# Optimization experiments

Hardware: AMD Instinct MI355X
Metric: run time of the kernel (lower is better)

Reference implementation:

```python
import jax, jax.numpy as jnp
import numpy as np

B, K, FM, TS, H, W = 128, 24, 24, 11, 40, 40
EPS = 1e-6


def setup_inputs() -> dict:
    key = jax.random.key(0)
    ks = jax.random.split(key, 8)

    def w(k, shape):
        fan_in = float(np.prod(shape[2:]))
        return jax.random.normal(k, shape, jnp.float32) / np.float32(np.sqrt(fan_in))

    return {
        "x": jax.random.normal(ks[0], (B, 1, H, W), jnp.float32),
        "noise": jax.random.uniform(ks[1], (B, K), jnp.float32, -2.0, 2.0),
        "W1": w(ks[2], (K, 128, 1, 3, 3)), "b1": jnp.zeros((K, 128), jnp.float32),
        "W2": w(ks[3], (K, 128, 128, 3, 3)), "b2": jnp.zeros((K, 128), jnp.float32),
        "W3": w(ks[4], (K, 128, 128, 3, 3)), "b3": jnp.zeros((K, 128), jnp.float32),
        "W4": w(ks[5], (K, 128, 128, 3, 3)), "b4": jnp.zeros((K, 128), jnp.float32),
        "W5": w(ks[6], (K, FM, 128, 1, 1)), "b5": jnp.zeros((K, FM), jnp.float32),
        "templates": jax.random.normal(ks[7], (K, TS, TS), jnp.float32),
    }


def _conv(x, w, b, s):
    y = jax.lax.conv_general_dilated(x, w, (s, s), 'VALID',
                                     dimension_numbers=('NCHW', 'OIHW', 'NCHW'))
    return y + b[None, :, None, None]


def _inv_affine_mats(pose):
    # pose [B,K,6]: angle(deg), tx, ty, scale, shear_x(deg), shear_y(deg)
    # torchvision-style inverse affine matrix (maps output canvas coords -> template coords)
    ang = jnp.deg2rad(pose[..., 0])
    tx, ty = pose[..., 1], pose[..., 2]
    sc = pose[..., 3] + EPS
    sx = jnp.deg2rad(pose[..., 4])
    sy = jnp.deg2rad(pose[..., 5])
    a = jnp.cos(ang - sy) / jnp.cos(sy)
    b = -jnp.cos(ang - sy) * jnp.tan(sx) / jnp.cos(sy) - jnp.sin(ang)
    c = jnp.sin(ang - sy) / jnp.cos(sy)
    d = -jnp.sin(ang - sy) * jnp.tan(sx) / jnp.cos(sy) + jnp.cos(ang)
    m00, m01, m10, m11 = d / sc, -b / sc, -c / sc, a / sc
    cx = cy = (TS - 1) * 0.5
    m02 = m00 * (-cx - tx) + m01 * (-cy - ty) + cx
    m12 = m10 * (-cx - tx) + m11 * (-cy - ty) + cy
    return m00, m01, m02, m10, m11, m12


def _warp_templates(templates, pose):
    # Fused affine warp + resize-to-(H,W), bilinear, zero fill (batched grid_sample).
    m00, m01, m02, m10, m11, m12 = _inv_affine_mats(pose)  # each [B,K]
    ys, xs = jnp.meshgrid(jnp.arange(H, dtype=jnp.float32),
                          jnp.arange(W, dtype=jnp.float32), indexing='ij')
    u = (xs + 0.5) * (TS / W) - 0.5  # output pixel -> template-canvas x
    v = (ys + 0.5) * (TS / H) - 0.5
    src_x = m00[..., None, None] * u + m01[..., None, None] * v + m02[..., None, None]
    src_y = m10[..., None, None] * u + m11[..., None, None] * v + m12[..., None, None]

    def sample(tmpl, sx_, sy_):  # tmpl [TS,TS]; sx_,sy_ [B,H,W]
        x0 = jnp.floor(sx_); y0 = jnp.floor(sy_)
        wx = sx_ - x0; wy = sy_ - y0
        x0i = x0.astype(jnp.int32); y0i = y0.astype(jnp.int32)

        def tap(yi, xi):
            ok = (xi >= 0) & (xi < TS) & (yi >= 0) & (yi < TS)
            val = tmpl[jnp.clip(yi, 0, TS - 1), jnp.clip(xi, 0, TS - 1)]
            return jnp.where(ok, val, 0.0)

        v00 = tap(y0i, x0i); v01 = tap(y0i, x0i + 1)
        v10 = tap(y0i + 1, x0i); v11 = tap(y0i + 1, x0i + 1)
        return (v00 * (1 - wx) + v01 * wx) * (1 - wy) + (v10 * (1 - wx) + v11 * wx) * wy

    return jax.vmap(sample, in_axes=(0, 1, 1), out_axes=1)(templates, src_x, src_y)  # [B,K,H,W]


def _forward(x, noise, W1, b1, W2, b2, W3, b3, W4, b4, W5, b5, templates):
    def capsule(w1, bb1, w2, bb2, w3, bb3, w4, bb4, w5, bb5):
        h = jax.nn.relu(_conv(x, w1, bb1, 2))
        h = jax.nn.relu(_conv(h, w2, bb2, 2))
        h = jax.nn.relu(_conv(h, w3, bb3, 1))
        h = jax.nn.relu(_conv(h, w4, bb4, 1))
        return _conv(h, w5, bb5, 1)

    outs = jax.vmap(capsule)(W1, b1, W2, b2, W3, b3, W4, b4, W5, b5)  # [K,B,FM,h,w]
    att = outs[:, :, -1]  # [K,B,h,w]
    hs, ws = att.shape[-2:]
    att = jax.nn.softmax(att.reshape(K, B, hs * ws), axis=-1).reshape(K, B, hs, ws)
    pooled = jnp.einsum('kbfhw,kbhw->bkf', outs[:, :, :-1], att)  # [B,K,FM-1]

    x_m = jax.nn.relu(pooled[:, :, :6])                        # [B,K,6] pose
    d_m = jax.nn.sigmoid(pooled[:, :, 6] + noise)[..., None]   # [B,K,1] presence
    c_z = jax.nn.relu(pooled[:, :, 7:])                        # [B,K,16]

    tt = _warp_templates(templates, x_m)                       # [B,K,H,W]
    mix_prob = jax.nn.softmax(d_m * tt.reshape(B, K, H * W), axis=2).reshape(B, K, H, W)

    std = jnp.std(x.reshape(B, 1, -1), axis=-1, ddof=1)[:, None]   # [B,1,1] (unbiased, as torch)
    mult = (1.0 / jnp.sqrt(std * 2.0 * jnp.pi))[..., None]         # [B,1,1,1] (as written in source)
    pmul = (-1.0 / (2.0 * std ** 2))[..., None]                    # [B,1,1,1]
    xd = jax.lax.stop_gradient(x)                                  # detach_x = x.data
    gaussians = mult * jnp.exp((xd - tt) ** 2 * pmul)              # [B,K,H,W]
    ll = jnp.log(jnp.sum(gaussians * mix_prob, axis=1)).sum((-1, -2)).mean()

    x_m_det = jax.lax.stop_gradient(x_m)
    d_m_det = jax.lax.stop_gradient(d_m)
    tmpl_det = jnp.broadcast_to(jax.lax.stop_gradient(templates).reshape(1, K, TS * TS),
                                (B, K, TS * TS))
    input_ocae = jnp.concatenate([d_m_det, x_m_det, tmpl_det, c_z], axis=-1)  # [B,K,144]
    return ll, input_ocae, x_m_det, d_m_det


def reference(x, noise, W1, b1, W2, b2, W3, b3, W4, b4, W5, b5, templates):
    return _forward(x, noise, W1, b1, W2, b2, W3, b3, W4, b4, W5, b5, templates)
```

## Files before the change

kernel.cpp:

```cpp
#include <hip/hip_runtime.h>
#include <math.h>

typedef __attribute__((ext_vector_type(8))) short bf16x8;
typedef __attribute__((ext_vector_type(4))) float f32x4;
typedef unsigned int uint32;
typedef unsigned short ushort;

namespace {
constexpr int KK = 24, BB = 128;

constexpr size_t SZ_W1P = (size_t)24 * 128 * 32 * 2;
constexpr size_t SZ_W5P = (size_t)24 * 32 * 128 * 2;
constexpr size_t SZ_WB  = (size_t)24 * 128 * 1152 * 2;
constexpr size_t OFF_W1P = 0;
constexpr size_t OFF_W5P = OFF_W1P + SZ_W1P;
constexpr size_t OFF_WB2 = OFF_W5P + SZ_W5P;
constexpr size_t OFF_WB3 = OFF_WB2 + SZ_WB;
constexpr size_t OFF_WB4 = OFF_WB3 + SZ_WB;
constexpr size_t OFF_TT  = OFF_WB4 + SZ_WB;
constexpr size_t SZ_TT   = (size_t)128 * 24 * 1600 * 2;
constexpr size_t OFF_SMAX = OFF_TT + SZ_TT;
constexpr size_t OFF_SDEN = OFF_SMAX + 12288;
constexpr size_t OFF_DM   = OFF_SDEN + 12288;
constexpr size_t OFF_PART = OFF_DM + 12288;

constexpr long long O_OCAE = 1;
constexpr long long O_XM   = O_OCAE + (long long)BB * KK * 144;
constexpr long long O_DM   = O_XM + (long long)BB * KK * 6;

constexpr int R1_SZ   = 80864;
constexpr int XIM_OFF = 0;
constexpr int H1T_OFF = 23104;
constexpr int XSB_OFF = 74464;
constexpr int H2S_OFF = 0;
constexpr int H3S_OFF = 0;
constexpr int H4B_OFF = 31392;
constexpr int OUTS_OFF = 0;
constexpr int ATT_OFF = 4800;
constexpr int PS_OFF  = 5000;
}

__device__ inline ushort f2bf(float f) {
  uint32 u = __builtin_bit_cast(uint32, f);
  u += 0x7fffu + ((u >> 16) & 1u);
  return (ushort)(u >> 16);
}
__device__ inline float bf2f(ushort u) {
  return __builtin_bit_cast(float, (uint32)u << 16);
}
__device__ inline uint32 cvtpk(float a, float b) {
  uint32 r;
  asm("v_cvt_pk_bf16_f32 %0, %1, %2" : "=v"(r) : "v"(a), "v"(b));
  return r;
}

__global__ __launch_bounds__(128) void k_w1p(const float* __restrict__ W1,
                                             const float* __restrict__ W5,
                                             ushort* __restrict__ W1p,
                                             ushort* __restrict__ W5p) {
  const int k = blockIdx.x, t = threadIdx.x;
  {
    ushort tmp[32];
    #pragma unroll
    for (int i = 0; i < 32; ++i) tmp[i] = 0;
    #pragma unroll
    for (int j = 0; j < 9; ++j) tmp[j] = f2bf(W1[(k * 128 + t) * 9 + j]);
    uint4* dp = (uint4*)(W1p + ((size_t)k * 128 + t) * 32);
    #pragma unroll
    for (int i = 0; i < 4; ++i) dp[i] = ((uint4*)tmp)[i];
  }
  if (t < 32) {
    ushort* dp = W5p + ((size_t)k * 32 + t) * 128;
    if (t < 24) {
      const float* sp = W5 + (size_t)k * 3072 + t * 128;
      for (int ci = 0; ci < 128; ++ci) dp[ci] = f2bf(sp[ci]);
    } else {
      for (int ci = 0; ci < 128; ++ci) dp[ci] = 0;
    }
  }
}

__global__ __launch_bounds__(256) void k_wp(
    const float* __restrict__ W2, const float* __restrict__ W3, const float* __restrict__ W4,
    ushort* __restrict__ W2p, ushort* __restrict__ W3p, ushort* __restrict__ W4p) {
  const int blk = blockIdx.x;
  const int sel = blk / 384;
  const int bb = blk - sel * 384;
  const float* src = (sel == 0) ? W2 : (sel == 1) ? W3 : W4;
  ushort* dst = (sel == 0) ? W2p : (sel == 1) ? W3p : W4p;
  const int k = bb >> 4;
  const int co = ((bb & 15) << 3) + (threadIdx.x >> 5);
  const int cil = threadIdx.x & 31;
  #pragma unroll
  for (int c = 0; c < 4; ++c) {
    const float* sp = src + ((size_t)(k * 128 + co) * 128 + c * 32 + cil) * 9;
    float v[9];
    #pragma unroll
    for (int j = 0; j < 9; ++j) v[j] = sp[j];
    ushort* dp = dst + (size_t)(k * 4 + c) * 9 * 128 * 32;
    #pragma unroll
    for (int j = 0; j < 9; ++j) dp[(j * 128 + co) * 32 + cil] = f2bf(v[j]);
  }
}

__device__ inline float tapf(const float* tm, int yi, int xi) {
  const bool ok = (xi >= 0) & (xi < 11) & (yi >= 0) & (yi < 11);
  const int yc = min(max(yi, 0), 10), xc = min(max(xi, 0), 10);
  const float v = tm[yc * 11 + xc];
  return ok ? v : 0.0f;
}

__global__ __launch_bounds__(256, 2) void k_tower(
    const float* __restrict__ x, const ushort* __restrict__ W1p, const float* __restrict__ b1,
    const ushort* __restrict__ W2p, const float* __restrict__ b2,
    const ushort* __restrict__ W3p, const float* __restrict__ b3,
    const ushort* __restrict__ W4p, const float* __restrict__ b4,
    const ushort* __restrict__ W5p, const float* __restrict__ b5,
    const float* __restrict__ noise, const float* __restrict__ templates,
    float* __restrict__ out, ushort* __restrict__ ttb,
    float* __restrict__ smax, float* __restrict__ sden, float* __restrict__ dmw)
{
  const int bi = blockIdx.x;
  const int blk = (bi & 7) * 192 + (bi >> 3);
  const int kb0 = blk * 2;
  const int k = kb0 >> 7;
  const int b0 = kb0 & 127;
  const int t = threadIdx.x;

  __shared__ __align__(16) char R1[R1_SZ];
  __shared__ float red[8];
  __shared__ float b5s[24];
  __shared__ float tm[121];

  ushort* xim = (ushort*)(R1 + XIM_OFF);
  ushort* h1T = (ushort*)(R1 + H1T_OFF);
  ushort* xsb = (ushort*)(R1 + XSB_OFF);
  ushort* h2s = (ushort*)(R1 + H2S_OFF);
  ushort* h3s = (ushort*)(R1 + H3S_OFF);
  ushort* h4b = (ushort*)(R1 + H4B_OFF);
  float*  outs_s = (float*)(R1 + OUTS_OFF);
  float*  att_s  = (float*)(R1 + ATT_OFF);
  float*  ps  = (float*)(R1 + PS_OFF);

  for (int i = t; i < 800; i += 256) {
    const int im = i / 400, j = i - im * 400;
    const float4 v = ((const float4*)(x + (size_t)(b0 + im) * 1600))[j];
    uint2 pk;
    pk.x = cvtpk(v.x, v.y);
    pk.y = cvtpk(v.z, v.w);
    *(uint2*)(xsb + im * 1600 + 4 * j) = pk;
  }
  __syncthreads();

  for (int f = t; f < 722; f += 256) {
    const int im = f / 361, fl = f - im * 361;
    const int py = fl / 19, px = fl - 19 * py;
    const ushort* bp = xsb + im * 1600 + py * 80 + px * 2;
    const uint32 t0 = bp[0], t1 = bp[1], t2 = bp[2];
    const uint32 t3 = bp[40], t4 = bp[41], t5 = bp[42];
    const uint32 t6 = bp[80], t7 = bp[81], t8 = bp[82];
    uint4* dp = (uint4*)(xim + (im * 361 + fl) * 16);
    dp[0] = make_uint4(t0 | (t1 << 16), t2 | (t3 << 16), t4 | (t5 << 16), t6 | (t7 << 16));
    dp[1] = make_uint4(t8, 0u, 0u, 0u);
  }

  const int w = t >> 6, lane = t & 63, r = lane & 15, s = lane >> 4;
  const int img = w >> 1;
  const int wi  = w & 1;
  const int m0  = wi * 64;

  ushort* xim_i = xim + img * 5776;
  ushort* h1T_i = h1T + img * 14440;
  ushort* h2s_i = h2s + img * 12960;
  ushort* h3s_i = h3s + img * 7840;
  ushort* h4b_i = h4b + img * 3400;

  {
    int pb[6]; bool vld[6];
    #pragma unroll
    for (int ni = 0; ni < 6; ++ni) {
      const int n = 16 * ni + r;
      const int py = n / 9, px = n - 9 * py;
      pb[ni] = 38 * py + 2 * px;
      vld[ni] = (n < 81);
    }

    f32x4 acc[4][6];
    #pragma unroll
    for (int mi = 0; mi < 4; ++mi)
      #pragma unroll
      for (int ni = 0; ni < 6; ++ni) acc[mi][ni] = (f32x4){0.f, 0.f, 0.f, 0.f};

    for (int c = 0; c < 4; ++c) {
      __syncthreads();
      {
        const bf16x8 a1 = *(const bf16x8*)(W1p + ((size_t)k * 128 + 32 * c + 16 * wi + r) * 32 + 8 * s);
        const int cil0 = 16 * wi + 4 * s;
        const float4 b1v = *(const float4*)(b1 + k * 128 + 32 * c + cil0);
        const bf16x8 bz = {};
        for (int nt = 0; nt < 23; ++nt) {
          const int n = nt * 16 + r;
          const int pos = (n < 361) ? n : 360;
          bf16x8 bv = *(const bf16x8*)(xim_i + pos * 16 + 8 * (s & 1));
          if (s >= 2) bv = bz;
          f32x4 cc = __builtin_amdgcn_mfma_f32_16x16x32_bf16(a1, bv, (f32x4){0.f, 0.f, 0.f, 0.f}, 0, 0, 0);
          if (n < 361) {
            uint2 pk;
            pk.x = cvtpk(fmaxf(cc[0] + b1v.x, 0.f), fmaxf(cc[1] + b1v.y, 0.f));
            pk.y = cvtpk(fmaxf(cc[2] + b1v.z, 0.f), fmaxf(cc[3] + b1v.w, 0.f));
            *(uint2*)(h1T_i + n * 40 + cil0) = pk;
          }
        }
      }
      __syncthreads();
      const ushort* Abase = W2p + ((((size_t)k * 4 + c) * 9) * 128 + m0 + r) * 32 + 8 * s;
      bf16x8 Ab[2][4];
      #pragma unroll
      for (int mi = 0; mi < 4; ++mi) Ab[0][mi] = *(const bf16x8*)(Abase + mi * 512);
      #pragma unroll
      for (int j = 0; j < 9; ++j) {
        if (j < 8) {
          #pragma unroll
          for (int mi = 0; mi < 4; ++mi)
            Ab[(j + 1) & 1][mi] = *(const bf16x8*)(Abase + (size_t)(j + 1) * 4096 + mi * 512);
        }
        const int off = (j / 3) * 19 + (j - 3 * (j / 3));
        bf16x8 Bv[6];
        #pragma unroll
        for (int ni = 0; ni < 6; ++ni) {
          const int pos = vld[ni] ? pb[ni] + off : 0;
          Bv[ni] = *(const bf16x8*)(h1T_i + pos * 40 + 8 * s);
        }
        #pragma unroll
        for (int mi = 0; mi < 4; ++mi)
          #pragma unroll
          for (int ni = 0; ni < 6; ++ni)
            acc[mi][ni] = __builtin_amdgcn_mfma_f32_16x16x32_bf16(Ab[j & 1][mi], Bv[ni], acc[mi][ni], 0, 0, 0);
      }
    }
    __syncthreads();
    #pragma unroll
    for (int mi = 0; mi < 4; ++mi) {
      const int co0 = m0 + 16 * mi + 4 * s;
      const float4 bv = *(const float4*)(b2 + k * 128 + co0);
      const int c2 = co0 >> 5, cil = co0 & 31;
      #pragma unroll
      for (int ni = 0; ni < 6; ++ni) {
        const int p = 16 * ni + r;
        if (p < 81) {
          uint2 pk;
          pk.x = cvtpk(fmaxf(acc[mi][ni][0] + bv.x, 0.f), fmaxf(acc[mi][ni][1] + bv.y, 0.f));
          pk.y = cvtpk(fmaxf(acc[mi][ni][2] + bv.z, 0.f), fmaxf(acc[mi][ni][3] + bv.w, 0.f));
          *(uint2*)(h2s_i + (c2 * 81 + p) * 40 + cil) = pk;
        }
      }
    }
  }
  __syncthreads();

  {
    int pb[4]; bool vld[4];
    #pragma unroll
    for (int ni = 0; ni < 4; ++ni) {
      const int n = 16 * ni + r;
      const int py = n / 7, px = n - 7 * py;
      pb[ni] = (9 * py + px) * 40;
      vld[ni] = (n < 49);
    }
    f32x4 acc[4][4];
    #pragma unroll
    for (int mi = 0; mi < 4; ++mi)
      #pragma unroll
      for (int ni = 0; ni < 4; ++ni) acc[mi][ni] = (f32x4){0.f, 0.f, 0.f, 0.f};

    for (int c = 0; c < 4; ++c) {
      const ushort* Abase = W3p + ((((size_t)k * 4 + c) * 9) * 128 + m0 + r) * 32 + 8 * s;
      bf16x8 Ab[2][4];
      #pragma unroll
      for (int mi = 0; mi < 4; ++mi) Ab[0][mi] = *(const bf16x8*)(Abase + mi * 512);
      #pragma unroll
      for (int j = 0; j < 9; ++j) {
        if (j < 8) {
          #pragma unroll
          for (int mi = 0; mi < 4; ++mi)
            Ab[(j + 1) & 1][mi] = *(const bf16x8*)(Abase + (size_t)(j + 1) * 4096 + mi * 512);
        }
        const int off40 = ((j / 3) * 9 + (j - 3 * (j / 3))) * 40;
        bf16x8 Bv[4];
        #pragma unroll
        for (int ni = 0; ni < 4; ++ni) {
          const int pos40 = vld[ni] ? pb[ni] : 0;
          Bv[ni] = *(const bf16x8*)(h2s_i + c * 3240 + pos40 + off40 + 8 * s);
        }
        #pragma unroll
        for (int mi = 0; mi < 4; ++mi)
          #pragma unroll
          for (int ni = 0; ni < 4; ++ni)
            acc[mi][ni] = __builtin_amdgcn_mfma_f32_16x16x32_bf16(Ab[j & 1][mi], Bv[ni], acc[mi][ni], 0, 0, 0);
      }
    }
    __syncthreads();
    #pragma unroll
    for (int mi = 0; mi < 4; ++mi) {
      const int co0 = m0 + 16 * mi + 4 * s;
      const float4 bv = *(const float4*)(b3 + k * 128 + co0);
      const int c2 = co0 >> 5, cil = co0 & 31;
      #pragma unroll
      for (int ni = 0; ni < 4; ++ni) {
        const int p = 16 * ni + r;
        if (p < 49) {
          uint2 pk;
          pk.x = cvtpk(fmaxf(acc[mi][ni][0] + bv.x, 0.f), fmaxf(acc[mi][ni][1] + bv.y, 0.f));
          pk.y = cvtpk(fmaxf(acc[mi][ni][2] + bv.z, 0.f), fmaxf(acc[mi][ni][3] + bv.w, 0.f));
          *(uint2*)(h3s_i + (c2 * 49 + p) * 40 + cil) = pk;
        }
      }
    }
    for (int i = t; i < 121; i += 256) tm[i] = templates[k * 121 + i];
  }
  __syncthreads();

  {
    int pb[2]; bool vld[2];
    #pragma unroll
    for (int ni = 0; ni < 2; ++ni) {
      const int n = 16 * ni + r;
      const int py = n / 5, px = n - 5 * py;
      pb[ni] = (7 * py + px) * 40;
      vld[ni] = (n < 25);
    }
    f32x4 acc[4][2];
    #pragma unroll
    for (int mi = 0; mi < 4; ++mi)
      #pragma unroll
      for (int ni = 0; ni < 2; ++ni) acc[mi][ni] = (f32x4){0.f, 0.f, 0.f, 0.f};

    for (int c = 0; c < 4; ++c) {
      const ushort* Abase = W4p + ((((size_t)k * 4 + c) * 9) * 128 + m0 + r) * 32 + 8 * s;
      bf16x8 Ab[2][4];
      #pragma unroll
      for (int mi = 0; mi < 4; ++mi) Ab[0][mi] = *(const bf16x8*)(Abase + mi * 512);
      #pragma unroll
      for (int j = 0; j < 9; ++j) {
        if (j < 8) {
          #pragma unroll
          for (int mi = 0; mi < 4; ++mi)
            Ab[(j + 1) & 1][mi] = *(const bf16x8*)(Abase + (size_t)(j + 1) * 4096 + mi * 512);
        }
        const int off40 = ((j / 3) * 7 + (j - 3 * (j / 3))) * 40;
        bf16x8 Bv[2];
        #pragma unroll
        for (int ni = 0; ni < 2; ++ni) {
          const int pos40 = vld[ni] ? pb[ni] : 0;
          Bv[ni] = *(const bf16x8*)(h3s_i + c * 1960 + pos40 + off40 + 8 * s);
        }
        #pragma unroll
        for (int mi = 0; mi < 4; ++mi)
          #pragma unroll
          for (int ni = 0; ni < 2; ++ni)
            acc[mi][ni] = __builtin_amdgcn_mfma_f32_16x16x32_bf16(Ab[j & 1][mi], Bv[ni], acc[mi][ni], 0, 0, 0);
      }
    }
    __syncthreads();
    #pragma unroll
    for (int mi = 0; mi < 4; ++mi) {
      const int co0 = m0 + 16 * mi + 4 * s;
      const float4 bv = *(const float4*)(b4 + k * 128 + co0);
      #pragma unroll
      for (int ni = 0; ni < 2; ++ni) {
        const int p = 16 * ni + r;
        if (p < 25) {
          uint2 pk;
          pk.x = cvtpk(fmaxf(acc[mi][ni][0] + bv.x, 0.f), fmaxf(acc[mi][ni][1] + bv.y, 0.f));
          pk.y = cvtpk(fmaxf(acc[mi][ni][2] + bv.z, 0.f), fmaxf(acc[mi][ni][3] + bv.w, 0.f));
          *(uint2*)(h4b_i + p * 136 + co0) = pk;
        }
      }
    }
    if (t < 24) b5s[t] = b5[k * 24 + t];
  }
  __syncthreads();

  {
    const int mt = wi;
    f32x4 acc5[2];
    acc5[0] = (f32x4){0.f, 0.f, 0.f, 0.f};
    acc5[1] = (f32x4){0.f, 0.f, 0.f, 0.f};
    const ushort* A5 = W5p + ((size_t)k * 32 + mt * 16 + r) * 128 + 8 * s;
    #pragma unroll
    for (int ks = 0; ks < 4; ++ks) {
      const bf16x8 a5 = *(const bf16x8*)(A5 + ks * 32);
      #pragma unroll
      for (int nt = 0; nt < 2; ++nt) {
        const int p = 16 * nt + r;
        const int pv = (p < 25) ? p : 0;
        const bf16x8 bv = *(const bf16x8*)(h4b_i + pv * 136 + ks * 32 + 8 * s);
        acc5[nt] = __builtin_amdgcn_mfma_f32_16x16x32_bf16(a5, bv, acc5[nt], 0, 0, 0);
      }
    }
    #pragma unroll
    for (int nt = 0; nt < 2; ++nt) {
      const int p = 16 * nt + r;
      if (p < 25) {
        #pragma unroll
        for (int rg = 0; rg < 4; ++rg) {
          const int fm = mt * 16 + 4 * s + rg;
          if (fm < 24) outs_s[img * 600 + fm * 25 + p] = acc5[nt][rg] + b5s[fm];
        }
      }
    }
  }
  __syncthreads();

  if (!(t & 64)) {
    const int im = t >> 7;
    const int tl = t & 63;
    float v = (tl < 25) ? outs_s[im * 600 + 575 + tl] : -1e30f;
    #pragma unroll
    for (int off = 32; off; off >>= 1) v = fmaxf(v, __shfl_xor(v, off));
    const float m = v;
    float e = (tl < 25) ? expf(outs_s[im * 600 + 575 + tl] - m) : 0.0f;
    float ss = e;
    #pragma unroll
    for (int off = 32; off; off >>= 1) ss += __shfl_xor(ss, off);
    if (tl < 25) att_s[im * 25 + tl] = e / ss;
  }
  __syncthreads();

  {
    const int im = t >> 7;
    const int tl = t & 127;
    if (tl < 23) {
      float v = 0.f;
      #pragma unroll
      for (int p = 0; p < 25; ++p) v = fmaf(outs_s[im * 600 + tl * 25 + p], att_s[im * 25 + p], v);
      ps[im * 23 + tl] = v;
    }
  }
  __syncthreads();

  float dmv[2];
  #pragma unroll
  for (int im = 0; im < 2; ++im) {
    const int idx = (b0 + im) * KK + k;
    const float dl = ps[im * 23 + 6] + noise[idx];
    dmv[im] = 1.0f / (1.0f + expf(-dl));
  }

  #pragma unroll
  for (int im = 0; im < 2; ++im) {
    const int idx = (b0 + im) * KK + k;
    if (t < 144) {
      float v;
      if (t == 0)       v = dmv[im];
      else if (t < 7)   v = fmaxf(ps[im * 23 + t - 1], 0.0f);
      else if (t < 128) v = tm[t - 7];
      else              v = fmaxf(ps[im * 23 + 7 + (t - 128)], 0.0f);
      out[O_OCAE + (size_t)idx * 144 + t] = v;
    }
    if (t < 6) out[O_XM + (size_t)idx * 6 + t] = fmaxf(ps[im * 23 + t], 0.0f);
    if (t == 0) out[O_DM + idx] = dmv[im];
  }

  const int im = t >> 7;
  const int tl = t & 127;
  const int idx = (b0 + im) * KK + k;
  const float dm = dmv[im];

  const float D2R = 0.017453292519943295f;
  const float ang = fmaxf(ps[im * 23 + 0], 0.0f) * D2R;
  const float tx = fmaxf(ps[im * 23 + 1], 0.0f), ty = fmaxf(ps[im * 23 + 2], 0.0f);
  const float sc = fmaxf(ps[im * 23 + 3], 0.0f) + 1e-6f;
  const float sxr = fmaxf(ps[im * 23 + 4], 0.0f) * D2R;
  const float syr = fmaxf(ps[im * 23 + 5], 0.0f) * D2R;
  const float cas = cosf(ang - syr), sas = sinf(ang - syr);
  const float csy = cosf(syr), tsx = tanf(sxr);
  const float a_ = cas / csy;
  const float b_ = -cas * tsx / csy - sinf(ang);
  const float c_ = sas / csy;
  const float d_ = -sas * tsx / csy + cosf(ang);
  const float m00 = d_ / sc, m01 = -b_ / sc, m10 = -c_ / sc, m11 = a_ / sc;
  const float m02 = m00 * (-5.0f - tx) + m01 * (-5.0f - ty) + 5.0f;
  const float m12 = m10 * (-5.0f - tx) + m11 * (-5.0f - ty) + 5.0f;

  const float S = 0.275f;
  float ttv[13];
  float lmax = -1e30f;
  #pragma unroll
  for (int i = 0; i < 13; ++i) {
    const int pix = tl + 128 * i;
    float val2 = 0.0f;
    if (pix < 1600) {
      const int py = pix / 40, px = pix - 40 * py;
      const float u = (px + 0.5f) * S - 0.5f;
      const float v = (py + 0.5f) * S - 0.5f;
      const float sx = m00 * u + m01 * v + m02;
      const float sy = m10 * u + m11 * v + m12;
      const float x0 = floorf(sx), y0 = floorf(sy);
      const float wx = sx - x0, wy = sy - y0;
      const int xi = (int)x0, yi = (int)y0;
      const float v00 = tapf(tm, yi, xi);
      const float v01 = tapf(tm, yi, xi + 1);
      const float v10 = tapf(tm, yi + 1, xi);
      const float v11 = tapf(tm, yi + 1, xi + 1);
      const float val = (v00 * (1.0f - wx) + v01 * wx) * (1.0f - wy) + (v10 * (1.0f - wx) + v11 * wx) * wy;
      const ushort tb = f2bf(val);
      val2 = bf2f(tb);
      ttb[(size_t)idx * 1600 + pix] = tb;
      lmax = fmaxf(lmax, dm * val2);
    }
    ttv[i] = val2;
  }

  #pragma unroll
  for (int off = 32; off; off >>= 1) lmax = fmaxf(lmax, __shfl_xor(lmax, off));
  if ((t & 63) == 0) red[t >> 6] = lmax;
  __syncthreads();
  const float m = fmaxf(red[2 * im], red[2 * im + 1]);
  float ls = 0.0f;
  #pragma unroll
  for (int i = 0; i < 13; ++i)
    if (tl + 128 * i < 1600) ls += expf(fmaf(dm, ttv[i], -m));
  #pragma unroll
  for (int off = 32; off; off >>= 1) ls += __shfl_xor(ls, off);
  __syncthreads();
  if ((t & 63) == 0) red[4 + (t >> 6)] = ls;
  __syncthreads();
  if ((t & 127) == 0) {
    smax[idx] = m;
    sden[idx] = red[4 + 2 * im] + red[5 + 2 * im];
    dmw[idx] = dm;
  }
}

__global__ __launch_bounds__(256) void k_ll(
    const float* __restrict__ x, const ushort* __restrict__ ttb,
    const float* __restrict__ smax, const float* __restrict__ sden,
    const float* __restrict__ dmw, float* __restrict__ part)
{
  const int b = blockIdx.x >> 2;
  const int chunk = blockIdx.x & 3;
  const int t = threadIdx.x;

  __shared__ __align__(16) float xs[1600];
  __shared__ float kd[24], km[24], ki[24];
  __shared__ float red[4], red2[4];

  for (int i = t; i < 400; i += 256)
    ((float4*)xs)[i] = ((const float4*)(x + (size_t)b * 1600))[i];
  if (t < 24) {
    kd[t] = dmw[b * 24 + t];
    km[t] = smax[b * 24 + t];
    ki[t] = 1.0f / sden[b * 24 + t];
  }
  __syncthreads();

  float s1 = 0.f, s2 = 0.f;
  for (int i = t; i < 1600; i += 256) { const float v = xs[i]; s1 += v; s2 = fmaf(v, v, s2); }
  #pragma unroll
  for (int off = 32; off; off >>= 1) { s1 += __shfl_xor(s1, off); s2 += __shfl_xor(s2, off); }
  if ((t & 63) == 0) { red[t >> 6] = s1; red2[t >> 6] = s2; }
  __syncthreads();
  s1 = red[0] + red[1] + red[2] + red[3];
  s2 = red2[0] + red2[1] + red2[2] + red2[3];
  const float var = (s2 - s1 * s1 * (1.0f / 1600.0f)) * (1.0f / 1599.0f);
  const float stdv = sqrtf(var);
  const float mult = 1.0f / sqrtf(stdv * 6.283185307179586f);
  const float pmul = -1.0f / (2.0f * stdv * stdv);

  const int p0 = chunk * 400;
  float ll = 0.0f;
  for (int ii = t; ii < 400; ii += 256) {
    const int pix = p0 + ii;
    const float xv = xs[pix];
    float sum = 0.0f;
    #pragma unroll 6
    for (int kk2 = 0; kk2 < 24; ++kk2) {
      const float tv = bf2f(ttb[(size_t)(b * 24 + kk2) * 1600 + pix]);
      const float dxv = xv - tv;
      sum += expf(fmaf(dxv * dxv, pmul, fmaf(kd[kk2], tv, -km[kk2]))) * ki[kk2];
    }
    ll += logf(mult * sum);
  }
  #pragma unroll
  for (int off = 32; off; off >>= 1) ll += __shfl_xor(ll, off);
  __syncthreads();
  if ((t & 63) == 0) red[t >> 6] = ll;
  __syncthreads();
  if (t == 0) part[blockIdx.x] = red[0] + red[1] + red[2] + red[3];
}

__global__ void k_final(const float* __restrict__ part, float* __restrict__ out)
{
  const int t = threadIdx.x;
  float v = part[t] + part[t + 256];
  #pragma unroll
  for (int off = 32; off; off >>= 1) v += __shfl_xor(v, off);
  __shared__ float red[4];
  if ((t & 63) == 0) red[t >> 6] = v;
  __syncthreads();
  if (t == 0) out[0] = (red[0] + red[1] + red[2] + red[3]) * (1.0f / 128.0f);
}

extern "C" void kernel_launch(void* const* d_in, const int* in_sizes, int n_in,
                              void* d_out, int out_size, void* d_ws, size_t ws_size,
                              hipStream_t stream)
{
  const float* x     = (const float*)d_in[0];
  const float* noise = (const float*)d_in[1];
  const float* W1    = (const float*)d_in[2];
  const float* b1    = (const float*)d_in[3];
  const float* W2    = (const float*)d_in[4];
  const float* b2    = (const float*)d_in[5];
  const float* W3    = (const float*)d_in[6];
  const float* b3    = (const float*)d_in[7];
  const float* W4    = (const float*)d_in[8];
  const float* b4    = (const float*)d_in[9];
  const float* W5    = (const float*)d_in[10];
  const float* b5    = (const float*)d_in[11];
  const float* tmpl  = (const float*)d_in[12];
  float* out = (float*)d_out;
  char* wsb = (char*)d_ws;

  ushort* W1p = (ushort*)(wsb + OFF_W1P);
  ushort* W5p = (ushort*)(wsb + OFF_W5P);
  ushort* W2p = (ushort*)(wsb + OFF_WB2);
  ushort* W3p = (ushort*)(wsb + OFF_WB3);
  ushort* W4p = (ushort*)(wsb + OFF_WB4);
  ushort* ttp  = (ushort*)(wsb + OFF_TT);
  float* smaxp = (float*)(wsb + OFF_SMAX);
  float* sdenp = (float*)(wsb + OFF_SDEN);
  float* dmp   = (float*)(wsb + OFF_DM);
  float* partp = (float*)(wsb + OFF_PART);

  k_w1p<<<24, 128, 0, stream>>>(W1, W5, W1p, W5p);
  k_wp<<<1152, 256, 0, stream>>>(W2, W3, W4, W2p, W3p, W4p);
  k_tower<<<KK * BB / 2, 256, 0, stream>>>(x, W1p, b1, W2p, b2, W3p, b3, W4p, b4,
                                           W5p, b5, noise, tmpl, out, ttp, smaxp, sdenp, dmp);
  k_ll<<<BB * 4, 256, 0, stream>>>(x, ttp, smaxp, sdenp, dmp, partp);
  k_final<<<1, 256, 0, stream>>>(partp, out);
}
```

Before: 271.4 us.

## Split tower kernel N-dimension across twice as many waves per block

Doubles k_tower's block size from 256 to 512 threads. Each image is now handled by four waves, split across output channels and across spatial tiles, instead of two, so per-wave accumulator and B-fragment counts halve across the conv2–conv5 MFMA stages. MFMA bursts are also wrapped with s_setprio to favour matrix issue. The intent is more latency hiding and better occupancy. In exchange, every wave reloads the same A (weight) fragments, adding redundant global/L2 traffic, and the reductions gain extra synchronisation.

```diff
diff --git a/kernel.cpp b/kernel.cpp
--- a/kernel.cpp
+++ b/kernel.cpp
@@ -110,7 +110,7 @@
   return ok ? v : 0.0f;
 }
 
-__global__ __launch_bounds__(256, 2) void k_tower(
+__global__ __launch_bounds__(512, 4) void k_tower(
     const float* __restrict__ x, const ushort* __restrict__ W1p, const float* __restrict__ b1,
     const ushort* __restrict__ W2p, const float* __restrict__ b2,
     const ushort* __restrict__ W3p, const float* __restrict__ b3,
@@ -128,7 +128,7 @@
   const int t = threadIdx.x;
 
   __shared__ __align__(16) char R1[R1_SZ];
-  __shared__ float red[8];
+  __shared__ float red[16];
   __shared__ float b5s[24];
   __shared__ float tm[121];
 
@@ -142,7 +142,7 @@
   float*  att_s  = (float*)(R1 + ATT_OFF);
   float*  ps  = (float*)(R1 + PS_OFF);
 
-  for (int i = t; i < 800; i += 256) {
+  for (int i = t; i < 800; i += 512) {
     const int im = i / 400, j = i - im * 400;
     const float4 v = ((const float4*)(x + (size_t)(b0 + im) * 1600))[j];
     uint2 pk;
@@ -152,7 +152,7 @@
   }
   __syncthreads();
 
-  for (int f = t; f < 722; f += 256) {
+  for (int f = t; f < 722; f += 512) {
     const int im = f / 361, fl = f - im * 361;
     const int py = fl / 19, px = fl - 19 * py;
     const ushort* bp = xsb + im * 1600 + py * 80 + px * 2;
@@ -165,8 +165,10 @@
   }
 
   const int w = t >> 6, lane = t & 63, r = lane & 15, s = lane >> 4;
-  const int img = w >> 1;
-  const int wi  = w & 1;
+  const int img = w >> 2;
+  const int sub = w & 3;
+  const int wi  = sub & 1;
+  const int nj  = sub >> 1;
   const int m0  = wi * 64;
 
   ushort* xim_i = xim + img * 5776;
@@ -176,20 +178,20 @@
   ushort* h4b_i = h4b + img * 3400;
 
   {
-    int pb[6]; bool vld[6];
-    #pragma unroll
-    for (int ni = 0; ni < 6; ++ni) {
-      const int n = 16 * ni + r;
+    int pb[3]; bool vld[3];
+    #pragma unroll
+    for (int ni = 0; ni < 3; ++ni) {
+      const int n = nj * 48 + 16 * ni + r;
       const int py = n / 9, px = n - 9 * py;
       pb[ni] = 38 * py + 2 * px;
       vld[ni] = (n < 81);
     }
 
-    f32x4 acc[4][6];
+    f32x4 acc[4][3];
     #pragma unroll
     for (int mi = 0; mi < 4; ++mi)
       #pragma unroll
-      for (int ni = 0; ni < 6; ++ni) acc[mi][ni] = (f32x4){0.f, 0.f, 0.f, 0.f};
+      for (int ni = 0; ni < 3; ++ni) acc[mi][ni] = (f32x4){0.f, 0.f, 0.f, 0.f};
 
     for (int c = 0; c < 4; ++c) {
       __syncthreads();
@@ -198,7 +200,8 @@
         const int cil0 = 16 * wi + 4 * s;
         const float4 b1v = *(const float4*)(b1 + k * 128 + 32 * c + cil0);
         const bf16x8 bz = {};
-        for (int nt = 0; nt < 23; ++nt) {
+        const int nt0 = nj ? 12 : 0, nt1 = nj ? 23 : 12;
+        for (int nt = nt0; nt < nt1; ++nt) {
           const int n = nt * 16 + r;
           const int pos = (n < 361) ? n : 360;
           bf16x8 bv = *(const bf16x8*)(xim_i + pos * 16 + 8 * (s & 1));
@@ -225,17 +228,19 @@
             Ab[(j + 1) & 1][mi] = *(const bf16x8*)(Abase + (size_t)(j + 1) * 4096 + mi * 512);
         }
         const int off = (j / 3) * 19 + (j - 3 * (j / 3));
-        bf16x8 Bv[6];
+        bf16x8 Bv[3];
         #pragma unroll
-        for (int ni = 0; ni < 6; ++ni) {
+        for (int ni = 0; ni < 3; ++ni) {
           const int pos = vld[ni] ? pb[ni] + off : 0;
           Bv[ni] = *(const bf16x8*)(h1T_i + pos * 40 + 8 * s);
         }
+        __builtin_amdgcn_s_setprio(1);
         #pragma unroll
         for (int mi = 0; mi < 4; ++mi)
           #pragma unroll
-          for (int ni = 0; ni < 6; ++ni)
+          for (int ni = 0; ni < 3; ++ni)
             acc[mi][ni] = __builtin_amdgcn_mfma_f32_16x16x32_bf16(Ab[j & 1][mi], Bv[ni], acc[mi][ni], 0, 0, 0);
+        __builtin_amdgcn_s_setprio(0);
       }
     }
     __syncthreads();
@@ -245,8 +250,8 @@
       const float4 bv = *(const float4*)(b2 + k * 128 + co0);
       const int c2 = co0 >> 5, cil = co0 & 31;
       #pragma unroll
-      for (int ni = 0; ni < 6; ++ni) {
-        const int p = 16 * ni + r;
+      for (int ni = 0; ni < 3; ++ni) {
+        const int p = nj * 48 + 16 * ni + r;
         if (p < 81) {
           uint2 pk;
           pk.x = cvtpk(fmaxf(acc[mi][ni][0] + bv.x, 0.f), fmaxf(acc[mi][ni][1] + bv.y, 0.f));
@@ -259,19 +264,19 @@
   __syncthreads();
 
   {
-    int pb[4]; bool vld[4];
-    #pragma unroll
-    for (int ni = 0; ni < 4; ++ni) {
-      const int n = 16 * ni + r;
+    int pb[2]; bool vld[2];
+    #pragma unroll
+    for (int ni = 0; ni < 2; ++ni) {
+      const int n = nj * 32 + 16 * ni + r;
       const int py = n / 7, px = n - 7 * py;
       pb[ni] = (9 * py + px) * 40;
       vld[ni] = (n < 49);
     }
-    f32x4 acc[4][4];
+    f32x4 acc[4][2];
     #pragma unroll
     for (int mi = 0; mi < 4; ++mi)
       #pragma unroll
-      for (int ni = 0; ni < 4; ++ni) acc[mi][ni] = (f32x4){0.f, 0.f, 0.f, 0.f};
+      for (int ni = 0; ni < 2; ++ni) acc[mi][ni] = (f32x4){0.f, 0.f, 0.f, 0.f};
 
     for (int c = 0; c < 4; ++c) {
       const ushort* Abase = W3p + ((((size_t)k * 4 + c) * 9) * 128 + m0 + r) * 32 + 8 * s;
@@ -286,17 +291,19 @@
             Ab[(j + 1) & 1][mi] = *(const bf16x8*)(Abase + (size_t)(j + 1) * 4096 + mi * 512);
         }
         const int off40 = ((j / 3) * 9 + (j - 3 * (j / 3))) * 40;
-        bf16x8 Bv[4];
+        bf16x8 Bv[2];
         #pragma unroll
-        for (int ni = 0; ni < 4; ++ni) {
+        for (int ni = 0; ni < 2; ++ni) {
           const int pos40 = vld[ni] ? pb[ni] : 0;
           Bv[ni] = *(const bf16x8*)(h2s_i + c * 3240 + pos40 + off40 + 8 * s);
         }
+        __builtin_amdgcn_s_setprio(1);
         #pragma unroll
         for (int mi = 0; mi < 4; ++mi)
           #pragma unroll
-          for (int ni = 0; ni < 4; ++ni)
+          for (int ni = 0; ni < 2; ++ni)
             acc[mi][ni] = __builtin_amdgcn_mfma_f32_16x16x32_bf16(Ab[j & 1][mi], Bv[ni], acc[mi][ni], 0, 0, 0);
+        __builtin_amdgcn_s_setprio(0);
       }
     }
     __syncthreads();
@@ -306,8 +313,8 @@
       const float4 bv = *(const float4*)(b3 + k * 128 + co0);
       const int c2 = co0 >> 5, cil = co0 & 31;
       #pragma unroll
-      for (int ni = 0; ni < 4; ++ni) {
-        const int p = 16 * ni + r;
+      for (int ni = 0; ni < 2; ++ni) {
+        const int p = nj * 32 + 16 * ni + r;
         if (p < 49) {
           uint2 pk;
           pk.x = cvtpk(fmaxf(acc[mi][ni][0] + bv.x, 0.f), fmaxf(acc[mi][ni][1] + bv.y, 0.f));
@@ -316,24 +323,17 @@
         }
       }
     }
-    for (int i = t; i < 121; i += 256) tm[i] = templates[k * 121 + i];
+    if (t < 121) tm[t] = templates[k * 121 + t];
   }
   __syncthreads();
 
   {
-    int pb[2]; bool vld[2];
-    #pragma unroll
-    for (int ni = 0; ni < 2; ++ni) {
-      const int n = 16 * ni + r;
-      const int py = n / 5, px = n - 5 * py;
-      pb[ni] = (7 * py + px) * 40;
-      vld[ni] = (n < 25);
-    }
-    f32x4 acc[4][2];
-    #pragma unroll
-    for (int mi = 0; mi < 4; ++mi)
-      #pragma unroll
-      for (int ni = 0; ni < 2; ++ni) acc[mi][ni] = (f32x4){0.f, 0.f, 0.f, 0.f};
+    const int n4 = nj * 16 + r;
+    const int py4 = n4 / 5, px4 = n4 - 5 * py4;
+    const int pb4 = (n4 < 25) ? (7 * py4 + px4) * 40 : 0;
+    f32x4 acc[4];
+    #pragma unroll
+    for (int mi = 0; mi < 4; ++mi) acc[mi] = (f32x4){0.f, 0.f, 0.f, 0.f};
 
     for (int c = 0; c < 4; ++c) {
       const ushort* Abase = W4p + ((((size_t)k * 4 + c) * 9) * 128 + m0 + r) * 32 + 8 * s;
@@ -348,17 +348,12 @@
             Ab[(j + 1) & 1][mi] = *(const bf16x8*)(Abase + (size_t)(j + 1) * 4096 + mi * 512);
         }
         const int off40 = ((j / 3) * 7 + (j - 3 * (j / 3))) * 40;
-        bf16x8 Bv[2];
-        #pragma unroll
-        for (int ni = 0; ni < 2; ++ni) {
-          const int pos40 = vld[ni] ? pb[ni] : 0;
-          Bv[ni] = *(const bf16x8*)(h3s_i + c * 1960 + pos40 + off40 + 8 * s);
-        }
+        const bf16x8 bv = *(const bf16x8*)(h3s_i + c * 1960 + pb4 + off40 + 8 * s);
+        __builtin_amdgcn_s_setprio(1);
         #pragma unroll
         for (int mi = 0; mi < 4; ++mi)
-          #pragma unroll
-          for (int ni = 0; ni < 2; ++ni)
-            acc[mi][ni] = __builtin_amdgcn_mfma_f32_16x16x32_bf16(Ab[j & 1][mi], Bv[ni], acc[mi][ni], 0, 0, 0);
+          acc[mi] = __builtin_amdgcn_mfma_f32_16x16x32_bf16(Ab[j & 1][mi], bv, acc[mi], 0, 0, 0);
+        __builtin_amdgcn_s_setprio(0);
       }
     }
     __syncthreads();
@@ -366,15 +361,12 @@
     for (int mi = 0; mi < 4; ++mi) {
       const int co0 = m0 + 16 * mi + 4 * s;
       const float4 bv = *(const float4*)(b4 + k * 128 + co0);
-      #pragma unroll
-      for (int ni = 0; ni < 2; ++ni) {
-        const int p = 16 * ni + r;
-        if (p < 25) {
-          uint2 pk;
-          pk.x = cvtpk(fmaxf(acc[mi][ni][0] + bv.x, 0.f), fmaxf(acc[mi][ni][1] + bv.y, 0.f));
-          pk.y = cvtpk(fmaxf(acc[mi][ni][2] + bv.z, 0.f), fmaxf(acc[mi][ni][3] + bv.w, 0.f));
-          *(uint2*)(h4b_i + p * 136 + co0) = pk;
-        }
+      const int p = nj * 16 + r;
+      if (p < 25) {
+        uint2 pk;
+        pk.x = cvtpk(fmaxf(acc[mi][0] + bv.x, 0.f), fmaxf(acc[mi][1] + bv.y, 0.f));
+        pk.y = cvtpk(fmaxf(acc[mi][2] + bv.z, 0.f), fmaxf(acc[mi][3] + bv.w, 0.f));
+        *(uint2*)(h4b_i + p * 136 + co0) = pk;
       }
     }
     if (t < 24) b5s[t] = b5[k * 24 + t];
@@ -382,54 +374,43 @@
   __syncthreads();
 
   {
-    const int mt = wi;
-    f32x4 acc5[2];
-    acc5[0] = (f32x4){0.f, 0.f, 0.f, 0.f};
-    acc5[1] = (f32x4){0.f, 0.f, 0.f, 0.f};
-    const ushort* A5 = W5p + ((size_t)k * 32 + mt * 16 + r) * 128 + 8 * s;
+    f32x4 acc5 = (f32x4){0.f, 0.f, 0.f, 0.f};
+    const ushort* A5 = W5p + ((size_t)k * 32 + wi * 16 + r) * 128 + 8 * s;
+    const int p = nj * 16 + r;
+    const int pv = (p < 25) ? p : 0;
     #pragma unroll
     for (int ks = 0; ks < 4; ++ks) {
       const bf16x8 a5 = *(const bf16x8*)(A5 + ks * 32);
-      #pragma unroll
-      for (int nt = 0; nt < 2; ++nt) {
-        const int p = 16 * nt + r;
-        const int pv = (p < 25) ? p : 0;
-        const bf16x8 bv = *(const bf16x8*)(h4b_i + pv * 136 + ks * 32 + 8 * s);
-        acc5[nt] = __builtin_amdgcn_mfma_f32_16x16x32_bf16(a5, bv, acc5[nt], 0, 0, 0);
-      }
-    }
-    #pragma unroll
-    for (int nt = 0; nt < 2; ++nt) {
-      const int p = 16 * nt + r;
-      if (p < 25) {
-        #pragma unroll
-        for (int rg = 0; rg < 4; ++rg) {
-          const int fm = mt * 16 + 4 * s + rg;
-          if (fm < 24) outs_s[img * 600 + fm * 25 + p] = acc5[nt][rg] + b5s[fm];
-        }
-      }
-    }
-  }
-  __syncthreads();
-
-  if (!(t & 64)) {
-    const int im = t >> 7;
-    const int tl = t & 63;
-    float v = (tl < 25) ? outs_s[im * 600 + 575 + tl] : -1e30f;
+      const bf16x8 bv = *(const bf16x8*)(h4b_i + pv * 136 + ks * 32 + 8 * s);
+      acc5 = __builtin_amdgcn_mfma_f32_16x16x32_bf16(a5, bv, acc5, 0, 0, 0);
+    }
+    if (p < 25) {
+      #pragma unroll
+      for (int rg = 0; rg < 4; ++rg) {
+        const int fm = wi * 16 + 4 * s + rg;
+        if (fm < 24) outs_s[img * 600 + fm * 25 + p] = acc5[rg] + b5s[fm];
+      }
+    }
+  }
+  __syncthreads();
+
+  if (sub == 0) {
+    const int im = img;
+    float v = (lane < 25) ? outs_s[im * 600 + 575 + lane] : -1e30f;
     #pragma unroll
     for (int off = 32; off; off >>= 1) v = fmaxf(v, __shfl_xor(v, off));
     const float m = v;
-    float e = (tl < 25) ? expf(outs_s[im * 600 + 575 + tl] - m) : 0.0f;
+    float e = (lane < 25) ? expf(outs_s[im * 600 + 575 + lane] - m) : 0.0f;
     float ss = e;
     #pragma unroll
     for (int off = 32; off; off >>= 1) ss += __shfl_xor(ss, off);
-    if (tl < 25) att_s[im * 25 + tl] = e / ss;
+    if (lane < 25) att_s[im * 25 + lane] = e / ss;
   }
   __syncthreads();
 
   {
-    const int im = t >> 7;
-    const int tl = t & 127;
+    const int im = t >> 8;
+    const int tl = t & 255;
     if (tl < 23) {
       float v = 0.f;
       #pragma unroll
@@ -442,28 +423,29 @@
   float dmv[2];
   #pragma unroll
   for (int im = 0; im < 2; ++im) {
-    const int idx = (b0 + im) * KK + k;
-    const float dl = ps[im * 23 + 6] + noise[idx];
+    const int idx2 = (b0 + im) * KK + k;
+    const float dl = ps[im * 23 + 6] + noise[idx2];
     dmv[im] = 1.0f / (1.0f + expf(-dl));
   }
 
-  #pragma unroll
-  for (int im = 0; im < 2; ++im) {
-    const int idx = (b0 + im) * KK + k;
-    if (t < 144) {
-      float v;
-      if (t == 0)       v = dmv[im];
-      else if (t < 7)   v = fmaxf(ps[im * 23 + t - 1], 0.0f);
-      else if (t < 128) v = tm[t - 7];
-      else              v = fmaxf(ps[im * 23 + 7 + (t - 128)], 0.0f);
-      out[O_OCAE + (size_t)idx * 144 + t] = v;
-    }
-    if (t < 6) out[O_XM + (size_t)idx * 6 + t] = fmaxf(ps[im * 23 + t], 0.0f);
-    if (t == 0) out[O_DM + idx] = dmv[im];
-  }
-
-  const int im = t >> 7;
-  const int tl = t & 127;
+  if (t < 288) {
+    const int im2 = t / 144, t2 = t - im2 * 144;
+    const int idx2 = (b0 + im2) * KK + k;
+    float v;
+    if (t2 == 0)       v = dmv[im2];
+    else if (t2 < 7)   v = fmaxf(ps[im2 * 23 + t2 - 1], 0.0f);
+    else if (t2 < 128) v = tm[t2 - 7];
+    else               v = fmaxf(ps[im2 * 23 + 7 + (t2 - 128)], 0.0f);
+    out[O_OCAE + (size_t)idx2 * 144 + t2] = v;
+  }
+  if (t < 12) {
+    const int im2 = t / 6;
+    out[O_XM + (size_t)((b0 + im2) * KK + k) * 6 + (t - im2 * 6)] = fmaxf(ps[im2 * 23 + t - im2 * 6], 0.0f);
+  }
+  if (t < 2) out[O_DM + (b0 + t) * KK + k] = dmv[t];
+
+  const int im = t >> 8;
+  const int tl = t & 255;
   const int idx = (b0 + im) * KK + k;
   const float dm = dmv[im];
 
@@ -484,11 +466,11 @@
   const float m12 = m10 * (-5.0f - tx) + m11 * (-5.0f - ty) + 5.0f;
 
   const float S = 0.275f;
-  float ttv[13];
+  float ttv[7];
   float lmax = -1e30f;
   #pragma unroll
-  for (int i = 0; i < 13; ++i) {
-    const int pix = tl + 128 * i;
+  for (int i = 0; i < 7; ++i) {
+    const int pix = tl + 256 * i;
     float val2 = 0.0f;
     if (pix < 1600) {
       const int py = pix / 40, px = pix - 40 * py;
@@ -514,21 +496,21 @@
 
   #pragma unroll
   for (int off = 32; off; off >>= 1) lmax = fmaxf(lmax, __shfl_xor(lmax, off));
-  if ((t & 63) == 0) red[t >> 6] = lmax;
-  __syncthreads();
-  const float m = fmaxf(red[2 * im], red[2 * im + 1]);
+  if (lane == 0) red[w] = lmax;
+  __syncthreads();
+  const float m = fmaxf(fmaxf(red[im * 4], red[im * 4 + 1]), fmaxf(red[im * 4 + 2], red[im * 4 + 3]));
   float ls = 0.0f;
   #pragma unroll
-  for (int i = 0; i < 13; ++i)
-    if (tl + 128 * i < 1600) ls += expf(fmaf(dm, ttv[i], -m));
+  for (int i = 0; i < 7; ++i)
+    if (tl + 256 * i < 1600) ls += expf(fmaf(dm, ttv[i], -m));
   #pragma unroll
   for (int off = 32; off; off >>= 1) ls += __shfl_xor(ls, off);
   __syncthreads();
-  if ((t & 63) == 0) red[4 + (t >> 6)] = ls;
-  __syncthreads();
-  if ((t & 127) == 0) {
+  if (lane == 0) red[8 + w] = ls;
+  __syncthreads();
+  if (tl == 0) {
     smax[idx] = m;
-    sden[idx] = red[4 + 2 * im] + red[5 + 2 * im];
+    sden[idx] = red[8 + im * 4] + red[9 + im * 4] + red[10 + im * 4] + red[11 + im * 4];
     dmw[idx] = dm;
   }
 }
@@ -635,7 +617,7 @@
 
   k_w1p<<<24, 128, 0, stream>>>(W1, W5, W1p, W5p);
   k_wp<<<1152, 256, 0, stream>>>(W2, W3, W4, W2p, W3p, W4p);
-  k_tower<<<KK * BB / 2, 256, 0, stream>>>(x, W1p, b1, W2p, b2, W3p, b3, W4p, b4,
+  k_tower<<<KK * BB / 2, 512, 0, stream>>>(x, W1p, b1, W2p, b2, W3p, b3, W4p, b4,
                                            W5p, b5, noise, tmpl, out, ttp, smaxp, sdenp, dmp);
   k_ll<<<BB * 4, 256, 0, stream>>>(x, ttp, smaxp, sdenp, dmp, partp);
   k_final<<<1, 256, 0, stream>>>(partp, out);
```

Result: slower. 358.4 us (+32.1%).
